# Kernel tuning notes

Measured on AMD Instinct MI355X. Metric: run time of the kernel, lower is better.

The kernel has to match this reference:

```python
import jax, jax.numpy as jnp
import numpy as np

N, IN_DIM, HIDDEN, L = 20000, 128, 256, 6
ALPHA = 0.1
EPS = 1e-5

def setup_inputs() -> dict:
    key = jax.random.key(0)
    ks = jax.random.split(key, 8)
    x = jax.random.normal(ks[0], (N, IN_DIM), dtype=jnp.float32)
    E = 320000
    src = jax.random.randint(ks[1], (E,), 0, N)
    dst = jax.random.randint(ks[2], (E,), 0, N)
    edge_index = jnp.stack([src, dst], axis=0)
    s = 1.0 / np.sqrt(IN_DIM)
    W_in = jax.random.normal(ks[3], (IN_DIM, HIDDEN), dtype=jnp.float32) * s
    b_in = jnp.zeros((HIDDEN,), dtype=jnp.float32)
    g_in = jnp.ones((HIDDEN,), dtype=jnp.float32)
    beta_in = jnp.zeros((HIDDEN,), dtype=jnp.float32)
    sc = 1.0 / np.sqrt(HIDDEN)
    Wc = jax.random.normal(ks[4], (L, HIDDEN, HIDDEN), dtype=jnp.float32) * sc
    bc = jnp.zeros((L, HIDDEN), dtype=jnp.float32)
    gc = jnp.ones((L, HIDDEN), dtype=jnp.float32)
    betac = jnp.zeros((L, HIDDEN), dtype=jnp.float32)
    return {"x": x, "edge_index": edge_index, "W_in": W_in, "b_in": b_in,
            "g_in": g_in, "beta_in": beta_in, "Wc": Wc, "bc": bc,
            "gc": gc, "betac": betac}

def _layer_norm(h, g, b):
    mu = jnp.mean(h, axis=-1, keepdims=True)
    var = jnp.mean((h - mu) ** 2, axis=-1, keepdims=True)
    return (h - mu) * jax.lax.rsqrt(var + EPS) * g + b

def _gcn_norm(edge_index, n):
    # add self loops (weight 1), symmetric normalization
    loop = jnp.arange(n, dtype=edge_index.dtype)
    row = jnp.concatenate([edge_index[0], loop])
    col = jnp.concatenate([edge_index[1], loop])
    w = jnp.ones((row.shape[0],), dtype=jnp.float32)
    deg = jax.ops.segment_sum(w, col, num_segments=n)
    dinv = jnp.where(deg > 0, jax.lax.rsqrt(deg), 0.0)
    norm = dinv[row] * w * dinv[col]
    return row, col, norm

def reference(x, edge_index, W_in, b_in, g_in, beta_in, Wc, bc, gc, betac):
    n = x.shape[0]
    row, col, norm = _gcn_norm(edge_index, n)
    # input block: Linear -> GELU -> LayerNorm (dropout = eval identity)
    h = _layer_norm(jax.nn.gelu(x @ W_in + b_in), g_in, beta_in)
    h0 = h
    xcur = h
    for l in range(L):
        z = xcur @ Wc[l]                              # [N, H]
        agg = jax.ops.segment_sum(z[row] * norm[:, None], col, num_segments=n)
        out = agg + bc[l]
        out = _layer_norm(jax.nn.gelu(out), gc[l], betac[l])
        hblend = (1.0 - ALPHA) * out + ALPHA * h0
        xcur = xcur + hblend
    return xcur
```

## Files before the change

### kernel.cpp

```cpp
#include <hip/hip_runtime.h>
#include <hip/hip_bf16.h>
#include <math.h>

#define HID 256
typedef __attribute__((ext_vector_type(8))) short s16x8;
typedef __attribute__((ext_vector_type(4))) float f32x4;

__device__ __forceinline__ ushort f2bf(float f){
    uint u = __float_as_uint(f);
    u += 0x7FFF + ((u>>16)&1);
    return (ushort)(u>>16);
}
__device__ __forceinline__ float bf2f(ushort b){
    return __uint_as_float(((uint)b)<<16);
}
__device__ __forceinline__ float4 bf4_to_f4(ushort4 u){
    return make_float4(bf2f(u.x), bf2f(u.y), bf2f(u.z), bf2f(u.w));
}

__device__ __forceinline__ float gelu_tanh(float x){
    float u = 0.7978845608028654f*(x + 0.044715f*x*x*x);
    float t = 1.0f - 2.0f/(1.0f + __expf(2.0f*u));
    return 0.5f*x*(1.0f+t);
}

__global__ void k_count(const int* __restrict__ dst, int* __restrict__ cnt, int E){
    int e = blockIdx.x*blockDim.x + threadIdx.x;
    if(e<E) atomicAdd(&cnt[dst[e]], 1);
}

__global__ __launch_bounds__(256) void k_scan1(const int* __restrict__ cnt,
    int* __restrict__ tsum, int* __restrict__ bsum, int N){
    __shared__ int sm[256];
    int t = threadIdx.x, b = blockIdx.x;
    int base = b*1024 + t*4;
    int c0=0,c1=0,c2=0,c3=0;
    if(base+3 < N){
        int4 c = *reinterpret_cast<const int4*>(&cnt[base]);
        c0=c.x; c1=c.y; c2=c.z; c3=c.w;
    }else{
        if(base  <N) c0=cnt[base];
        if(base+1<N) c1=cnt[base+1];
        if(base+2<N) c2=cnt[base+2];
        if(base+3<N) c3=cnt[base+3];
    }
    int s = c0+c1+c2+c3;
    sm[t]=s; __syncthreads();
    for(int off=1; off<256; off<<=1){
        int v = sm[t];
        int a = (t>=off)? sm[t-off] : 0;
        __syncthreads();
        sm[t] = v+a;
        __syncthreads();
    }
    tsum[b*256+t] = sm[t]-s;
    if(t==255) bsum[b] = sm[255];
}

__global__ void k_scan2(const int* __restrict__ bsum, int* __restrict__ boff,
    int* __restrict__ indptr, int B, int N){
    if(threadIdx.x==0 && blockIdx.x==0){
        int run=0;
        for(int i=0;i<B;i++){ boff[i]=run; run+=bsum[i]; }
        indptr[N]=run;
    }
}

__global__ __launch_bounds__(256) void k_scan3(const int* __restrict__ cnt,
    const int* __restrict__ tsum, const int* __restrict__ boff,
    int* __restrict__ indptr, int* __restrict__ cursor, float* __restrict__ dinv, int N){
    int t = threadIdx.x, b = blockIdx.x;
    int base = b*1024 + t*4;
    int run = boff[b] + tsum[b*256+t];
    #pragma unroll
    for(int i=0;i<4;i++){
        int idx = base+i;
        if(idx<N){
            int c = cnt[idx];
            indptr[idx]=run; cursor[idx]=run;
            dinv[idx] = rsqrtf((float)(c+1));
            run += c;
        }
    }
}

__global__ void k_fill(const int* __restrict__ src, const int* __restrict__ dst,
    int* __restrict__ cursor, int* __restrict__ csr, int E){
    int e = blockIdx.x*blockDim.x + threadIdx.x;
    if(e<E){
        int pos = atomicAdd(&cursor[dst[e]], 1);
        csr[pos] = src[e];
    }
}

__global__ void k_cvt(const float* __restrict__ in, ushort* __restrict__ out, int total4){
    int i = blockIdx.x*blockDim.x + threadIdx.x;
    if(i < total4){
        float4 v = reinterpret_cast<const float4*>(in)[i];
        ushort4 o; o.x=f2bf(v.x); o.y=f2bf(v.y); o.z=f2bf(v.z); o.w=f2bf(v.w);
        reinterpret_cast<ushort4*>(out)[i] = o;
    }
}

__global__ void k_cvt_win(const float* __restrict__ W, ushort* __restrict__ Wb){
    int i = blockIdx.x*blockDim.x + threadIdx.x;
    if(i >= 128*256) return;
    int k = i >> 8, n = i & 255;
    int kb = k>>5, hi=(k>>3)&3, ii=k&7;
    Wb[((kb*256+n)*4+hi)*8 + ii] = f2bf(W[i]);
}
__global__ void k_cvt_wc(const float* __restrict__ W, ushort* __restrict__ Wb){
    int i = blockIdx.x*blockDim.x + threadIdx.x;
    if(i >= 6*65536) return;
    int l = i >> 16;
    int k = (i>>8)&255, n = i&255;
    int kb = k>>5, hi=(k>>3)&3, ii=k&7;
    Wb[l*65536 + ((kb*256+n)*4+hi)*8 + ii] = f2bf(W[i]);
}

__global__ __launch_bounds__(256) void k_agg(const ushort* __restrict__ xsc,
    const int* __restrict__ indptr, const int* __restrict__ csr,
    const float* __restrict__ dinv, ushort* __restrict__ yb, int N)
{
    int wave = threadIdx.x>>6, lane = threadIdx.x&63;
    int n = blockIdx.x*4 + wave;
    if(n>=N) return;
    const ushort4* X4 = reinterpret_cast<const ushort4*>(xsc);
    float4 acc = bf4_to_f4(X4[(size_t)n*64+lane]);
    int e0 = indptr[n], e1 = indptr[n+1];
    int e = e0;
    for(; e+4<=e1; e+=4){
        int i0=csr[e], i1=csr[e+1], i2=csr[e+2], i3=csr[e+3];
        float4 v0 = bf4_to_f4(X4[(size_t)i0*64+lane]);
        float4 v1 = bf4_to_f4(X4[(size_t)i1*64+lane]);
        float4 v2 = bf4_to_f4(X4[(size_t)i2*64+lane]);
        float4 v3 = bf4_to_f4(X4[(size_t)i3*64+lane]);
        acc.x += (v0.x+v1.x)+(v2.x+v3.x);
        acc.y += (v0.y+v1.y)+(v2.y+v3.y);
        acc.z += (v0.z+v1.z)+(v2.z+v3.z);
        acc.w += (v0.w+v1.w)+(v2.w+v3.w);
    }
    for(; e<e1; e++){
        float4 v = bf4_to_f4(X4[(size_t)csr[e]*64+lane]);
        acc.x+=v.x; acc.y+=v.y; acc.z+=v.z; acc.w+=v.w;
    }
    float dn = dinv[n];
    ushort4 o; o.x=f2bf(dn*acc.x); o.y=f2bf(dn*acc.y); o.z=f2bf(dn*acc.z); o.w=f2bf(dn*acc.w);
    reinterpret_cast<ushort4*>(yb)[(size_t)n*64+lane] = o;
}

template<int K, bool INPUT>
__global__ __launch_bounds__(256) void k_gemm_fused(const ushort* __restrict__ A,
    const ushort* __restrict__ Wb,
    const float* __restrict__ bp, const float* __restrict__ gp, const float* __restrict__ bep,
    const float* __restrict__ dinv, ushort* __restrict__ h0b,
    float* __restrict__ xcur, ushort* __restrict__ xsc, int N)
{
    constexpr int KB = K/32;
    const int lane = threadIdx.x & 63;
    const int wc = threadIdx.x >> 6;
    const int lr = lane & 15;
    const int hi = lane >> 4;
    const int row0 = blockIdx.x*32;

    f32x4 acc[2][4];
    #pragma unroll
    for(int m=0;m<2;m++)
        #pragma unroll
        for(int n=0;n<4;n++){ acc[m][n].x=0.f; acc[m][n].y=0.f; acc[m][n].z=0.f; acc[m][n].w=0.f; }

    int r0 = row0 + lr;      if(r0 >= N) r0 = N-1;
    int r1 = row0 + 16 + lr; if(r1 >= N) r1 = N-1;
    const ushort* ap0 = A + (size_t)r0*K + hi*8;
    const ushort* ap1 = A + (size_t)r1*K + hi*8;
    const ushort* bpp = Wb + (wc*64 + lr)*32 + hi*8;

    s16x8 a0[2], a1[2], bb[2][4];
    a0[0] = *reinterpret_cast<const s16x8*>(ap0);
    a1[0] = *reinterpret_cast<const s16x8*>(ap1);
    #pragma unroll
    for(int nf=0;nf<4;nf++) bb[0][nf] = *reinterpret_cast<const s16x8*>(bpp + nf*512);

    #pragma unroll
    for(int kb=0; kb<KB; kb++){
        const int cur = kb&1, nxt = cur^1;
        if(kb+1 < KB){
            a0[nxt] = *reinterpret_cast<const s16x8*>(ap0 + (kb+1)*32);
            a1[nxt] = *reinterpret_cast<const s16x8*>(ap1 + (kb+1)*32);
            #pragma unroll
            for(int nf=0;nf<4;nf++)
                bb[nxt][nf] = *reinterpret_cast<const s16x8*>(bpp + (kb+1)*8192 + nf*512);
        }
        #pragma unroll
        for(int nf=0;nf<4;nf++){
            acc[0][nf] = __builtin_amdgcn_mfma_f32_16x16x32_bf16(a0[cur], bb[cur][nf], acc[0][nf], 0,0,0);
            acc[1][nf] = __builtin_amdgcn_mfma_f32_16x16x32_bf16(a1[cur], bb[cur][nf], acc[1][nf], 0,0,0);
        }
    }

    float bcv[4], gcv[4], bev[4];
    #pragma unroll
    for(int nf=0;nf<4;nf++){
        int col = wc*64 + nf*16 + lr;
        bcv[nf]=bp[col]; gcv[nf]=gp[col]; bev[nf]=bep[col];
    }
    __shared__ float sm1[32][4];
    __shared__ float sm2[32][4];
    #pragma unroll
    for(int m=0;m<2;m++){
        #pragma unroll
        for(int r=0;r<4;r++){
            float ls1=0.f, ls2=0.f;
            #pragma unroll
            for(int nf=0;nf<4;nf++){
                float t = gelu_tanh(acc[m][nf][r] + bcv[nf]);
                acc[m][nf][r] = t;
                ls1 += t; ls2 += t*t;
            }
            #pragma unroll
            for(int off=1; off<16; off<<=1){
                ls1 += __shfl_xor(ls1, off, 64);
                ls2 += __shfl_xor(ls2, off, 64);
            }
            if(lr==0){
                int row = m*16 + hi*4 + r;
                sm1[row][wc]=ls1; sm2[row][wc]=ls2;
            }
        }
    }
    __syncthreads();
    #pragma unroll
    for(int m=0;m<2;m++){
        #pragma unroll
        for(int r=0;r<4;r++){
            int row = m*16 + hi*4 + r;
            int grow = row0 + row;
            if(grow >= N) continue;
            float S1 = sm1[row][0]+sm1[row][1]+sm1[row][2]+sm1[row][3];
            float S2 = sm2[row][0]+sm2[row][1]+sm2[row][2]+sm2[row][3];
            float mu = S1*(1.0f/256.0f);
            float var = fmaxf(S2*(1.0f/256.0f) - mu*mu, 0.0f);
            float rs = rsqrtf(var + 1e-5f);
            float dv = dinv[grow];
            #pragma unroll
            for(int nf=0;nf<4;nf++){
                int col = wc*64 + nf*16 + lr;
                size_t idx = (size_t)grow*HID + col;
                float o = (acc[m][nf][r]-mu)*rs*gcv[nf] + bev[nf];
                if(INPUT){
                    h0b[idx] = f2bf(o);
                    xcur[idx] = o;
                    xsc[idx] = f2bf(dv*o);
                }else{
                    float h = bf2f(h0b[idx]);
                    float xc = xcur[idx] + 0.9f*o + 0.1f*h;
                    xcur[idx] = xc;
                    xsc[idx] = f2bf(dv*xc);
                }
            }
        }
    }
}

extern "C" void kernel_launch(void* const* d_in, const int* in_sizes, int n_in,
                              void* d_out, int out_size, void* d_ws, size_t ws_size,
                              hipStream_t stream){
    const float* x     = (const float*)d_in[0];
    const int*   ei    = (const int*)d_in[1];
    const float* W_in  = (const float*)d_in[2];
    const float* b_in  = (const float*)d_in[3];
    const float* g_in  = (const float*)d_in[4];
    const float* be_in = (const float*)d_in[5];
    const float* Wc    = (const float*)d_in[6];
    const float* bc    = (const float*)d_in[7];
    const float* gc    = (const float*)d_in[8];
    const float* bec   = (const float*)d_in[9];
    const int N = in_sizes[0]/128;
    const int E = in_sizes[1]/2;
    const int* src = ei;
    const int* dst = ei + E;
    float* xcur = (float*)d_out;
    const int B = (N+1023)/1024;

    char* w = (char*)d_ws;
    ushort* xsc  = (ushort*)w; w += (size_t)N*HID*2;
    ushort* yb   = (ushort*)w; w += (size_t)N*HID*2;
    ushort* h0b  = (ushort*)w; w += (size_t)N*HID*2;
    ushort* xin  = (ushort*)w; w += (size_t)N*128*2;
    ushort* wbin = (ushort*)w; w += (size_t)128*256*2;
    ushort* wbc  = (ushort*)w; w += (size_t)6*65536*2;
    float* dinv  = (float*)w;  w += (size_t)N*4;
    int* cnt     = (int*)w;    w += (size_t)N*4;
    int* cursor  = (int*)w;    w += (size_t)N*4;
    int* csr     = (int*)w;    w += (size_t)E*4;
    int* indptr  = (int*)w;    w += (size_t)(N+1)*4;
    int* tsum    = (int*)w;    w += (size_t)B*256*4;
    int* bsum    = (int*)w;    w += (size_t)B*4;
    int* boff    = (int*)w;    w += (size_t)B*4;

    hipMemsetAsync(cnt, 0, (size_t)N*4, stream);
    k_count<<<(E+255)/256,256,0,stream>>>(dst,cnt,E);
    k_scan1<<<B,256,0,stream>>>(cnt, tsum, bsum, N);
    k_scan2<<<1,64,0,stream>>>(bsum, boff, indptr, B, N);
    k_scan3<<<B,256,0,stream>>>(cnt, tsum, boff, indptr, cursor, dinv, N);
    k_fill<<<(E+255)/256,256,0,stream>>>(src,dst,cursor,csr,E);

    k_cvt<<<((N*128/4)+255)/256,256,0,stream>>>(x, xin, N*128/4);
    k_cvt_win<<<(128*256+255)/256,256,0,stream>>>(W_in, wbin);
    k_cvt_wc<<<(6*65536+255)/256,256,0,stream>>>(Wc, wbc);

    const int GB = (N+31)/32;
    k_gemm_fused<128,true><<<GB,256,0,stream>>>(xin, wbin, b_in, g_in, be_in,
                                                dinv, h0b, xcur, xsc, N);
    for(int l=0;l<6;l++){
        k_agg<<<(N+3)/4,256,0,stream>>>(xsc, indptr, csr, dinv, yb, N);
        k_gemm_fused<256,false><<<GB,256,0,stream>>>(yb, wbc+(size_t)l*65536,
            bc+(size_t)l*HID, gc+(size_t)l*HID, bec+(size_t)l*HID,
            dinv, h0b, xcur, xsc, N);
    }
}
```

Measured before the change: 361.7 us.

## Fuse neighbor aggregation into the per-layer GEMM via LDS staging

Merges the CSR gather-aggregation kernel into the layer GEMM. Each block aggregates its 32 rows into swizzled shared memory, then runs MFMA directly from LDS, with ping-pong feature buffers between layers. The fp32-to-bf16 conversion of the input features is also folded into the input GEMM. This removes the intermediate aggregated-feature round trip through global memory, seven launches and one conversion pass. In exchange, far fewer waves are available to hide the latency of the irregular gather, since each wave now walks 8 nodes serially.

```diff
diff --git a/kernel.cpp b/kernel.cpp
--- a/kernel.cpp
+++ b/kernel.cpp
@@ -93,15 +93,6 @@
     }
 }
 
-__global__ void k_cvt(const float* __restrict__ in, ushort* __restrict__ out, int total4){
-    int i = blockIdx.x*blockDim.x + threadIdx.x;
-    if(i < total4){
-        float4 v = reinterpret_cast<const float4*>(in)[i];
-        ushort4 o; o.x=f2bf(v.x); o.y=f2bf(v.y); o.z=f2bf(v.z); o.w=f2bf(v.w);
-        reinterpret_cast<ushort4*>(out)[i] = o;
-    }
-}
-
 __global__ void k_cvt_win(const float* __restrict__ W, ushort* __restrict__ Wb){
     int i = blockIdx.x*blockDim.x + threadIdx.x;
     if(i >= 128*256) return;
@@ -118,94 +109,20 @@
     Wb[l*65536 + ((kb*256+n)*4+hi)*8 + ii] = f2bf(W[i]);
 }
 
-__global__ __launch_bounds__(256) void k_agg(const ushort* __restrict__ xsc,
-    const int* __restrict__ indptr, const int* __restrict__ csr,
-    const float* __restrict__ dinv, ushort* __restrict__ yb, int N)
-{
-    int wave = threadIdx.x>>6, lane = threadIdx.x&63;
-    int n = blockIdx.x*4 + wave;
-    if(n>=N) return;
-    const ushort4* X4 = reinterpret_cast<const ushort4*>(xsc);
-    float4 acc = bf4_to_f4(X4[(size_t)n*64+lane]);
-    int e0 = indptr[n], e1 = indptr[n+1];
-    int e = e0;
-    for(; e+4<=e1; e+=4){
-        int i0=csr[e], i1=csr[e+1], i2=csr[e+2], i3=csr[e+3];
-        float4 v0 = bf4_to_f4(X4[(size_t)i0*64+lane]);
-        float4 v1 = bf4_to_f4(X4[(size_t)i1*64+lane]);
-        float4 v2 = bf4_to_f4(X4[(size_t)i2*64+lane]);
-        float4 v3 = bf4_to_f4(X4[(size_t)i3*64+lane]);
-        acc.x += (v0.x+v1.x)+(v2.x+v3.x);
-        acc.y += (v0.y+v1.y)+(v2.y+v3.y);
-        acc.z += (v0.z+v1.z)+(v2.z+v3.z);
-        acc.w += (v0.w+v1.w)+(v2.w+v3.w);
-    }
-    for(; e<e1; e++){
-        float4 v = bf4_to_f4(X4[(size_t)csr[e]*64+lane]);
-        acc.x+=v.x; acc.y+=v.y; acc.z+=v.z; acc.w+=v.w;
-    }
-    float dn = dinv[n];
-    ushort4 o; o.x=f2bf(dn*acc.x); o.y=f2bf(dn*acc.y); o.z=f2bf(dn*acc.z); o.w=f2bf(dn*acc.w);
-    reinterpret_cast<ushort4*>(yb)[(size_t)n*64+lane] = o;
-}
-
-template<int K, bool INPUT>
-__global__ __launch_bounds__(256) void k_gemm_fused(const ushort* __restrict__ A,
-    const ushort* __restrict__ Wb,
+template<bool INPUT>
+__device__ __forceinline__ void epilogue(f32x4 (&acc)[2][4],
     const float* __restrict__ bp, const float* __restrict__ gp, const float* __restrict__ bep,
     const float* __restrict__ dinv, ushort* __restrict__ h0b,
-    float* __restrict__ xcur, ushort* __restrict__ xsc, int N)
+    float* __restrict__ xcur, ushort* __restrict__ xs_out,
+    int row0, int wc, int lr, int hi, int N,
+    float (*sm1)[4], float (*sm2)[4])
 {
-    constexpr int KB = K/32;
-    const int lane = threadIdx.x & 63;
-    const int wc = threadIdx.x >> 6;
-    const int lr = lane & 15;
-    const int hi = lane >> 4;
-    const int row0 = blockIdx.x*32;
-
-    f32x4 acc[2][4];
-    #pragma unroll
-    for(int m=0;m<2;m++)
-        #pragma unroll
-        for(int n=0;n<4;n++){ acc[m][n].x=0.f; acc[m][n].y=0.f; acc[m][n].z=0.f; acc[m][n].w=0.f; }
-
-    int r0 = row0 + lr;      if(r0 >= N) r0 = N-1;
-    int r1 = row0 + 16 + lr; if(r1 >= N) r1 = N-1;
-    const ushort* ap0 = A + (size_t)r0*K + hi*8;
-    const ushort* ap1 = A + (size_t)r1*K + hi*8;
-    const ushort* bpp = Wb + (wc*64 + lr)*32 + hi*8;
-
-    s16x8 a0[2], a1[2], bb[2][4];
-    a0[0] = *reinterpret_cast<const s16x8*>(ap0);
-    a1[0] = *reinterpret_cast<const s16x8*>(ap1);
-    #pragma unroll
-    for(int nf=0;nf<4;nf++) bb[0][nf] = *reinterpret_cast<const s16x8*>(bpp + nf*512);
-
-    #pragma unroll
-    for(int kb=0; kb<KB; kb++){
-        const int cur = kb&1, nxt = cur^1;
-        if(kb+1 < KB){
-            a0[nxt] = *reinterpret_cast<const s16x8*>(ap0 + (kb+1)*32);
-            a1[nxt] = *reinterpret_cast<const s16x8*>(ap1 + (kb+1)*32);
-            #pragma unroll
-            for(int nf=0;nf<4;nf++)
-                bb[nxt][nf] = *reinterpret_cast<const s16x8*>(bpp + (kb+1)*8192 + nf*512);
-        }
-        #pragma unroll
-        for(int nf=0;nf<4;nf++){
-            acc[0][nf] = __builtin_amdgcn_mfma_f32_16x16x32_bf16(a0[cur], bb[cur][nf], acc[0][nf], 0,0,0);
-            acc[1][nf] = __builtin_amdgcn_mfma_f32_16x16x32_bf16(a1[cur], bb[cur][nf], acc[1][nf], 0,0,0);
-        }
-    }
-
     float bcv[4], gcv[4], bev[4];
     #pragma unroll
     for(int nf=0;nf<4;nf++){
         int col = wc*64 + nf*16 + lr;
         bcv[nf]=bp[col]; gcv[nf]=gp[col]; bev[nf]=bep[col];
     }
-    __shared__ float sm1[32][4];
-    __shared__ float sm2[32][4];
     #pragma unroll
     for(int m=0;m<2;m++){
         #pragma unroll
@@ -250,16 +167,144 @@
                 if(INPUT){
                     h0b[idx] = f2bf(o);
                     xcur[idx] = o;
-                    xsc[idx] = f2bf(dv*o);
+                    xs_out[idx] = f2bf(dv*o);
                 }else{
                     float h = bf2f(h0b[idx]);
                     float xc = xcur[idx] + 0.9f*o + 0.1f*h;
                     xcur[idx] = xc;
-                    xsc[idx] = f2bf(dv*xc);
+                    xs_out[idx] = f2bf(dv*xc);
                 }
             }
         }
     }
+}
+
+__global__ __launch_bounds__(256) void k_gemm_in(const float* __restrict__ X,
+    const ushort* __restrict__ Wb,
+    const float* __restrict__ bp, const float* __restrict__ gp, const float* __restrict__ bep,
+    const float* __restrict__ dinv, ushort* __restrict__ h0b,
+    float* __restrict__ xcur, ushort* __restrict__ xs_out, int N)
+{
+    const int lane = threadIdx.x & 63;
+    const int wc = threadIdx.x >> 6;
+    const int lr = lane & 15;
+    const int hi = lane >> 4;
+    const int row0 = blockIdx.x*32;
+    __shared__ float sm1[32][4];
+    __shared__ float sm2[32][4];
+
+    f32x4 acc[2][4];
+    #pragma unroll
+    for(int m=0;m<2;m++)
+        #pragma unroll
+        for(int n=0;n<4;n++){ acc[m][n].x=0.f; acc[m][n].y=0.f; acc[m][n].z=0.f; acc[m][n].w=0.f; }
+
+    int r0 = row0 + lr;      if(r0 >= N) r0 = N-1;
+    int r1 = row0 + 16 + lr; if(r1 >= N) r1 = N-1;
+    const float* xp0 = X + (size_t)r0*128 + hi*8;
+    const float* xp1 = X + (size_t)r1*128 + hi*8;
+    const ushort* bpp = Wb + (wc*64 + lr)*32 + hi*8;
+
+    #pragma unroll
+    for(int kb=0; kb<4; kb++){
+        float4 p0a = *reinterpret_cast<const float4*>(xp0 + kb*32);
+        float4 p0b = *reinterpret_cast<const float4*>(xp0 + kb*32 + 4);
+        float4 p1a = *reinterpret_cast<const float4*>(xp1 + kb*32);
+        float4 p1b = *reinterpret_cast<const float4*>(xp1 + kb*32 + 4);
+        s16x8 a0, a1;
+        a0[0]=(short)f2bf(p0a.x); a0[1]=(short)f2bf(p0a.y); a0[2]=(short)f2bf(p0a.z); a0[3]=(short)f2bf(p0a.w);
+        a0[4]=(short)f2bf(p0b.x); a0[5]=(short)f2bf(p0b.y); a0[6]=(short)f2bf(p0b.z); a0[7]=(short)f2bf(p0b.w);
+        a1[0]=(short)f2bf(p1a.x); a1[1]=(short)f2bf(p1a.y); a1[2]=(short)f2bf(p1a.z); a1[3]=(short)f2bf(p1a.w);
+        a1[4]=(short)f2bf(p1b.x); a1[5]=(short)f2bf(p1b.y); a1[6]=(short)f2bf(p1b.z); a1[7]=(short)f2bf(p1b.w);
+        #pragma unroll
+        for(int nf=0;nf<4;nf++){
+            s16x8 b = *reinterpret_cast<const s16x8*>(bpp + kb*8192 + nf*512);
+            acc[0][nf] = __builtin_amdgcn_mfma_f32_16x16x32_bf16(a0, b, acc[0][nf], 0,0,0);
+            acc[1][nf] = __builtin_amdgcn_mfma_f32_16x16x32_bf16(a1, b, acc[1][nf], 0,0,0);
+        }
+    }
+    epilogue<true>(acc, bp, gp, bep, dinv, h0b, xcur, xs_out, row0, wc, lr, hi, N, sm1, sm2);
+}
+
+__global__ __launch_bounds__(256) void k_conv(const ushort* __restrict__ xs_in,
+    const ushort* __restrict__ Wb,
+    const int* __restrict__ indptr, const int* __restrict__ csr,
+    const float* __restrict__ dinv,
+    const float* __restrict__ bp, const float* __restrict__ gp, const float* __restrict__ bep,
+    ushort* __restrict__ h0b, float* __restrict__ xcur,
+    ushort* __restrict__ xs_out, int N)
+{
+    __shared__ ushort yls[32*256];
+    __shared__ float sm1[32][4];
+    __shared__ float sm2[32][4];
+    const int lane = threadIdx.x & 63;
+    const int wc = threadIdx.x >> 6;
+    const int lr = lane & 15;
+    const int hi = lane >> 4;
+    const int row0 = blockIdx.x*32;
+
+    const ushort4* X4 = reinterpret_cast<const ushort4*>(xs_in);
+    char* ybase = (char*)yls;
+    #pragma unroll 1
+    for(int i=0;i<8;i++){
+        int li = wc*8 + i;
+        int n = row0 + li;
+        if(n >= N) n = N-1;
+        float4 acc = bf4_to_f4(X4[(size_t)n*64 + lane]);
+        int e0 = indptr[n], e1 = indptr[n+1];
+        int e = e0;
+        for(; e+4<=e1; e+=4){
+            int i0=csr[e], i1=csr[e+1], i2=csr[e+2], i3=csr[e+3];
+            float4 v0 = bf4_to_f4(X4[(size_t)i0*64+lane]);
+            float4 v1 = bf4_to_f4(X4[(size_t)i1*64+lane]);
+            float4 v2 = bf4_to_f4(X4[(size_t)i2*64+lane]);
+            float4 v3 = bf4_to_f4(X4[(size_t)i3*64+lane]);
+            acc.x += (v0.x+v1.x)+(v2.x+v3.x);
+            acc.y += (v0.y+v1.y)+(v2.y+v3.y);
+            acc.z += (v0.z+v1.z)+(v2.z+v3.z);
+            acc.w += (v0.w+v1.w)+(v2.w+v3.w);
+        }
+        for(; e<e1; e++){
+            float4 v = bf4_to_f4(X4[(size_t)csr[e]*64+lane]);
+            acc.x+=v.x; acc.y+=v.y; acc.z+=v.z; acc.w+=v.w;
+        }
+        float dn = dinv[n];
+        ushort4 o; o.x=f2bf(dn*acc.x); o.y=f2bf(dn*acc.y); o.z=f2bf(dn*acc.z); o.w=f2bf(dn*acc.w);
+        *reinterpret_cast<ushort4*>(ybase + li*512 + ((lane*8) ^ ((li&7)<<4))) = o;
+    }
+    __syncthreads();
+
+    f32x4 acc[2][4];
+    #pragma unroll
+    for(int m=0;m<2;m++)
+        #pragma unroll
+        for(int n=0;n<4;n++){ acc[m][n].x=0.f; acc[m][n].y=0.f; acc[m][n].z=0.f; acc[m][n].w=0.f; }
+
+    const ushort* bpp = Wb + (wc*64 + lr)*32 + hi*8;
+    s16x8 bb[2][4];
+    #pragma unroll
+    for(int nf=0;nf<4;nf++) bb[0][nf] = *reinterpret_cast<const s16x8*>(bpp + nf*512);
+
+    const int sws = (lr&7)<<4;
+    #pragma unroll
+    for(int kb=0; kb<8; kb++){
+        const int cur = kb&1, nxt = cur^1;
+        if(kb < 7){
+            #pragma unroll
+            for(int nf=0;nf<4;nf++)
+                bb[nxt][nf] = *reinterpret_cast<const s16x8*>(bpp + (kb+1)*8192 + nf*512);
+        }
+        int cb = kb*64 + hi*16;
+        s16x8 a0 = *reinterpret_cast<const s16x8*>(ybase + lr*512        + (cb ^ sws));
+        s16x8 a1 = *reinterpret_cast<const s16x8*>(ybase + (16+lr)*512   + (cb ^ sws));
+        #pragma unroll
+        for(int nf=0;nf<4;nf++){
+            acc[0][nf] = __builtin_amdgcn_mfma_f32_16x16x32_bf16(a0, bb[cur][nf], acc[0][nf], 0,0,0);
+            acc[1][nf] = __builtin_amdgcn_mfma_f32_16x16x32_bf16(a1, bb[cur][nf], acc[1][nf], 0,0,0);
+        }
+    }
+    __syncthreads();
+    epilogue<false>(acc, bp, gp, bep, dinv, h0b, xcur, xs_out, row0, wc, lr, hi, N, sm1, sm2);
 }
 
 extern "C" void kernel_launch(void* const* d_in, const int* in_sizes, int n_in,
@@ -283,10 +328,9 @@
     const int B = (N+1023)/1024;
 
     char* w = (char*)d_ws;
-    ushort* xsc  = (ushort*)w; w += (size_t)N*HID*2;
-    ushort* yb   = (ushort*)w; w += (size_t)N*HID*2;
+    ushort* xs0  = (ushort*)w; w += (size_t)N*HID*2;
+    ushort* xs1  = (ushort*)w; w += (size_t)N*HID*2;
     ushort* h0b  = (ushort*)w; w += (size_t)N*HID*2;
-    ushort* xin  = (ushort*)w; w += (size_t)N*128*2;
     ushort* wbin = (ushort*)w; w += (size_t)128*256*2;
     ushort* wbc  = (ushort*)w; w += (size_t)6*65536*2;
     float* dinv  = (float*)w;  w += (size_t)N*4;
@@ -298,24 +342,24 @@
     int* bsum    = (int*)w;    w += (size_t)B*4;
     int* boff    = (int*)w;    w += (size_t)B*4;
 
-    hipMemsetAsync(cnt, 0, (size_t)N*4, stream);
+    (void)hipMemsetAsync(cnt, 0, (size_t)N*4, stream);
     k_count<<<(E+255)/256,256,0,stream>>>(dst,cnt,E);
     k_scan1<<<B,256,0,stream>>>(cnt, tsum, bsum, N);
     k_scan2<<<1,64,0,stream>>>(bsum, boff, indptr, B, N);
     k_scan3<<<B,256,0,stream>>>(cnt, tsum, boff, indptr, cursor, dinv, N);
     k_fill<<<(E+255)/256,256,0,stream>>>(src,dst,cursor,csr,E);
 
-    k_cvt<<<((N*128/4)+255)/256,256,0,stream>>>(x, xin, N*128/4);
     k_cvt_win<<<(128*256+255)/256,256,0,stream>>>(W_in, wbin);
     k_cvt_wc<<<(6*65536+255)/256,256,0,stream>>>(Wc, wbc);
 
     const int GB = (N+31)/32;
-    k_gemm_fused<128,true><<<GB,256,0,stream>>>(xin, wbin, b_in, g_in, be_in,
-                                                dinv, h0b, xcur, xsc, N);
+    k_gemm_in<<<GB,256,0,stream>>>(x, wbin, b_in, g_in, be_in, dinv, h0b, xcur, xs0, N);
+    ushort* xsA = xs0;
+    ushort* xsB = xs1;
     for(int l=0;l<6;l++){
-        k_agg<<<(N+3)/4,256,0,stream>>>(xsc, indptr, csr, dinv, yb, N);
-        k_gemm_fused<256,false><<<GB,256,0,stream>>>(yb, wbc+(size_t)l*65536,
+        k_conv<<<GB,256,0,stream>>>(xsA, wbc+(size_t)l*65536, indptr, csr, dinv,
             bc+(size_t)l*HID, gc+(size_t)l*HID, bec+(size_t)l*HID,
-            dinv, h0b, xcur, xsc, N);
-    }
-}
+            h0b, xcur, xsB, N);
+        ushort* t = xsA; xsA = xsB; xsB = t;
+    }
+}
```

New measurement: 410.4 us. +13.5%, slower.

## Fuse input conversion into GEMM, halve GEMM row tile, unroll aggregation by eight

Applied to the files above, without the earlier changes.

Drops the separate fp32-to-bf16 conversion kernel for x; the input GEMM now reads fp32 rows and converts them in registers. Both fused GEMM kernels now handle 16 rows per block instead of 32, which doubles the grid size and reuses each weight fragment load across fewer rows, with the epilogue moved into a shared helper. The aggregation loop issues eight gathers at a time instead of four to put more loads in flight. Smaller tiles increase weight traffic per row, and the wider unroll adds register pressure.

```diff
diff --git a/kernel.cpp b/kernel.cpp
--- a/kernel.cpp
+++ b/kernel.cpp
@@ -93,15 +93,6 @@
     }
 }
 
-__global__ void k_cvt(const float* __restrict__ in, ushort* __restrict__ out, int total4){
-    int i = blockIdx.x*blockDim.x + threadIdx.x;
-    if(i < total4){
-        float4 v = reinterpret_cast<const float4*>(in)[i];
-        ushort4 o; o.x=f2bf(v.x); o.y=f2bf(v.y); o.z=f2bf(v.z); o.w=f2bf(v.w);
-        reinterpret_cast<ushort4*>(out)[i] = o;
-    }
-}
-
 __global__ void k_cvt_win(const float* __restrict__ W, ushort* __restrict__ Wb){
     int i = blockIdx.x*blockDim.x + threadIdx.x;
     if(i >= 128*256) return;
@@ -129,7 +120,19 @@
     float4 acc = bf4_to_f4(X4[(size_t)n*64+lane]);
     int e0 = indptr[n], e1 = indptr[n+1];
     int e = e0;
-    for(; e+4<=e1; e+=4){
+    for(; e+8<=e1; e+=8){
+        int idx[8];
+        #pragma unroll
+        for(int q=0;q<8;q++) idx[q]=csr[e+q];
+        float4 v[8];
+        #pragma unroll
+        for(int q=0;q<8;q++) v[q]=bf4_to_f4(X4[(size_t)idx[q]*64+lane]);
+        #pragma unroll
+        for(int q=0;q<8;q++){
+            acc.x+=v[q].x; acc.y+=v[q].y; acc.z+=v[q].z; acc.w+=v[q].w;
+        }
+    }
+    if(e+4<=e1){
         int i0=csr[e], i1=csr[e+1], i2=csr[e+2], i3=csr[e+3];
         float4 v0 = bf4_to_f4(X4[(size_t)i0*64+lane]);
         float4 v1 = bf4_to_f4(X4[(size_t)i1*64+lane]);
@@ -139,6 +142,7 @@
         acc.y += (v0.y+v1.y)+(v2.y+v3.y);
         acc.z += (v0.z+v1.z)+(v2.z+v3.z);
         acc.w += (v0.w+v1.w)+(v2.w+v3.w);
+        e += 4;
     }
     for(; e<e1; e++){
         float4 v = bf4_to_f4(X4[(size_t)csr[e]*64+lane]);
@@ -149,117 +153,149 @@
     reinterpret_cast<ushort4*>(yb)[(size_t)n*64+lane] = o;
 }
 
-template<int K, bool INPUT>
+template<bool INPUT>
+__device__ __forceinline__ void epilogue16(f32x4 (&acc)[4],
+    const float* __restrict__ bp, const float* __restrict__ gp, const float* __restrict__ bep,
+    const float* __restrict__ dinv, ushort* __restrict__ h0b,
+    float* __restrict__ xcur, ushort* __restrict__ xs_out,
+    int row0, int wc, int lr, int hi, int N,
+    float (*sm1)[4], float (*sm2)[4])
+{
+    float bcv[4], gcv[4], bev[4];
+    #pragma unroll
+    for(int nf=0;nf<4;nf++){
+        int col = wc*64 + nf*16 + lr;
+        bcv[nf]=bp[col]; gcv[nf]=gp[col]; bev[nf]=bep[col];
+    }
+    #pragma unroll
+    for(int r=0;r<4;r++){
+        float ls1=0.f, ls2=0.f;
+        #pragma unroll
+        for(int nf=0;nf<4;nf++){
+            float t = gelu_tanh(acc[nf][r] + bcv[nf]);
+            acc[nf][r] = t;
+            ls1 += t; ls2 += t*t;
+        }
+        #pragma unroll
+        for(int off=1; off<16; off<<=1){
+            ls1 += __shfl_xor(ls1, off, 64);
+            ls2 += __shfl_xor(ls2, off, 64);
+        }
+        if(lr==0){
+            int row = hi*4 + r;
+            sm1[row][wc]=ls1; sm2[row][wc]=ls2;
+        }
+    }
+    __syncthreads();
+    #pragma unroll
+    for(int r=0;r<4;r++){
+        int row = hi*4 + r;
+        int grow = row0 + row;
+        if(grow >= N) continue;
+        float S1 = sm1[row][0]+sm1[row][1]+sm1[row][2]+sm1[row][3];
+        float S2 = sm2[row][0]+sm2[row][1]+sm2[row][2]+sm2[row][3];
+        float mu = S1*(1.0f/256.0f);
+        float var = fmaxf(S2*(1.0f/256.0f) - mu*mu, 0.0f);
+        float rs = rsqrtf(var + 1e-5f);
+        float dv = dinv[grow];
+        #pragma unroll
+        for(int nf=0;nf<4;nf++){
+            int col = wc*64 + nf*16 + lr;
+            size_t idx = (size_t)grow*HID + col;
+            float o = (acc[nf][r]-mu)*rs*gcv[nf] + bev[nf];
+            if(INPUT){
+                h0b[idx] = f2bf(o);
+                xcur[idx] = o;
+                xs_out[idx] = f2bf(dv*o);
+            }else{
+                float h = bf2f(h0b[idx]);
+                float xc = xcur[idx] + 0.9f*o + 0.1f*h;
+                xcur[idx] = xc;
+                xs_out[idx] = f2bf(dv*xc);
+            }
+        }
+    }
+}
+
+__global__ __launch_bounds__(256) void k_gemm_in(const float* __restrict__ X,
+    const ushort* __restrict__ Wb,
+    const float* __restrict__ bp, const float* __restrict__ gp, const float* __restrict__ bep,
+    const float* __restrict__ dinv, ushort* __restrict__ h0b,
+    float* __restrict__ xcur, ushort* __restrict__ xs_out, int N)
+{
+    const int lane = threadIdx.x & 63;
+    const int wc = threadIdx.x >> 6;
+    const int lr = lane & 15;
+    const int hi = lane >> 4;
+    const int row0 = blockIdx.x*16;
+    __shared__ float sm1[16][4];
+    __shared__ float sm2[16][4];
+
+    f32x4 acc[4];
+    #pragma unroll
+    for(int n=0;n<4;n++){ acc[n].x=0.f; acc[n].y=0.f; acc[n].z=0.f; acc[n].w=0.f; }
+
+    int r0 = row0 + lr; if(r0 >= N) r0 = N-1;
+    const float* xp0 = X + (size_t)r0*128 + hi*8;
+    const ushort* bpp = Wb + (wc*64 + lr)*32 + hi*8;
+
+    #pragma unroll
+    for(int kb=0; kb<4; kb++){
+        float4 p0a = *reinterpret_cast<const float4*>(xp0 + kb*32);
+        float4 p0b = *reinterpret_cast<const float4*>(xp0 + kb*32 + 4);
+        s16x8 a0;
+        a0[0]=(short)f2bf(p0a.x); a0[1]=(short)f2bf(p0a.y); a0[2]=(short)f2bf(p0a.z); a0[3]=(short)f2bf(p0a.w);
+        a0[4]=(short)f2bf(p0b.x); a0[5]=(short)f2bf(p0b.y); a0[6]=(short)f2bf(p0b.z); a0[7]=(short)f2bf(p0b.w);
+        #pragma unroll
+        for(int nf=0;nf<4;nf++){
+            s16x8 b = *reinterpret_cast<const s16x8*>(bpp + kb*8192 + nf*512);
+            acc[nf] = __builtin_amdgcn_mfma_f32_16x16x32_bf16(a0, b, acc[nf], 0,0,0);
+        }
+    }
+    epilogue16<true>(acc, bp, gp, bep, dinv, h0b, xcur, xs_out, row0, wc, lr, hi, N, sm1, sm2);
+}
+
 __global__ __launch_bounds__(256) void k_gemm_fused(const ushort* __restrict__ A,
     const ushort* __restrict__ Wb,
     const float* __restrict__ bp, const float* __restrict__ gp, const float* __restrict__ bep,
     const float* __restrict__ dinv, ushort* __restrict__ h0b,
-    float* __restrict__ xcur, ushort* __restrict__ xsc, int N)
+    float* __restrict__ xcur, ushort* __restrict__ xs_out, int N)
 {
-    constexpr int KB = K/32;
     const int lane = threadIdx.x & 63;
     const int wc = threadIdx.x >> 6;
     const int lr = lane & 15;
     const int hi = lane >> 4;
-    const int row0 = blockIdx.x*32;
-
-    f32x4 acc[2][4];
-    #pragma unroll
-    for(int m=0;m<2;m++)
-        #pragma unroll
-        for(int n=0;n<4;n++){ acc[m][n].x=0.f; acc[m][n].y=0.f; acc[m][n].z=0.f; acc[m][n].w=0.f; }
-
-    int r0 = row0 + lr;      if(r0 >= N) r0 = N-1;
-    int r1 = row0 + 16 + lr; if(r1 >= N) r1 = N-1;
-    const ushort* ap0 = A + (size_t)r0*K + hi*8;
-    const ushort* ap1 = A + (size_t)r1*K + hi*8;
+    const int row0 = blockIdx.x*16;
+    __shared__ float sm1[16][4];
+    __shared__ float sm2[16][4];
+
+    f32x4 acc[4];
+    #pragma unroll
+    for(int n=0;n<4;n++){ acc[n].x=0.f; acc[n].y=0.f; acc[n].z=0.f; acc[n].w=0.f; }
+
+    int r0 = row0 + lr; if(r0 >= N) r0 = N-1;
+    const ushort* ap0 = A + (size_t)r0*256 + hi*8;
     const ushort* bpp = Wb + (wc*64 + lr)*32 + hi*8;
 
-    s16x8 a0[2], a1[2], bb[2][4];
+    s16x8 a0[2], bb[2][4];
     a0[0] = *reinterpret_cast<const s16x8*>(ap0);
-    a1[0] = *reinterpret_cast<const s16x8*>(ap1);
     #pragma unroll
     for(int nf=0;nf<4;nf++) bb[0][nf] = *reinterpret_cast<const s16x8*>(bpp + nf*512);
 
     #pragma unroll
-    for(int kb=0; kb<KB; kb++){
+    for(int kb=0; kb<8; kb++){
         const int cur = kb&1, nxt = cur^1;
-        if(kb+1 < KB){
+        if(kb < 7){
             a0[nxt] = *reinterpret_cast<const s16x8*>(ap0 + (kb+1)*32);
-            a1[nxt] = *reinterpret_cast<const s16x8*>(ap1 + (kb+1)*32);
             #pragma unroll
             for(int nf=0;nf<4;nf++)
                 bb[nxt][nf] = *reinterpret_cast<const s16x8*>(bpp + (kb+1)*8192 + nf*512);
         }
         #pragma unroll
-        for(int nf=0;nf<4;nf++){
-            acc[0][nf] = __builtin_amdgcn_mfma_f32_16x16x32_bf16(a0[cur], bb[cur][nf], acc[0][nf], 0,0,0);
-            acc[1][nf] = __builtin_amdgcn_mfma_f32_16x16x32_bf16(a1[cur], bb[cur][nf], acc[1][nf], 0,0,0);
-        }
-    }
-
-    float bcv[4], gcv[4], bev[4];
-    #pragma unroll
-    for(int nf=0;nf<4;nf++){
-        int col = wc*64 + nf*16 + lr;
-        bcv[nf]=bp[col]; gcv[nf]=gp[col]; bev[nf]=bep[col];
-    }
-    __shared__ float sm1[32][4];
-    __shared__ float sm2[32][4];
-    #pragma unroll
-    for(int m=0;m<2;m++){
-        #pragma unroll
-        for(int r=0;r<4;r++){
-            float ls1=0.f, ls2=0.f;
-            #pragma unroll
-            for(int nf=0;nf<4;nf++){
-                float t = gelu_tanh(acc[m][nf][r] + bcv[nf]);
-                acc[m][nf][r] = t;
-                ls1 += t; ls2 += t*t;
-            }
-            #pragma unroll
-            for(int off=1; off<16; off<<=1){
-                ls1 += __shfl_xor(ls1, off, 64);
-                ls2 += __shfl_xor(ls2, off, 64);
-            }
-            if(lr==0){
-                int row = m*16 + hi*4 + r;
-                sm1[row][wc]=ls1; sm2[row][wc]=ls2;
-            }
-        }
-    }
-    __syncthreads();
-    #pragma unroll
-    for(int m=0;m<2;m++){
-        #pragma unroll
-        for(int r=0;r<4;r++){
-            int row = m*16 + hi*4 + r;
-            int grow = row0 + row;
-            if(grow >= N) continue;
-            float S1 = sm1[row][0]+sm1[row][1]+sm1[row][2]+sm1[row][3];
-            float S2 = sm2[row][0]+sm2[row][1]+sm2[row][2]+sm2[row][3];
-            float mu = S1*(1.0f/256.0f);
-            float var = fmaxf(S2*(1.0f/256.0f) - mu*mu, 0.0f);
-            float rs = rsqrtf(var + 1e-5f);
-            float dv = dinv[grow];
-            #pragma unroll
-            for(int nf=0;nf<4;nf++){
-                int col = wc*64 + nf*16 + lr;
-                size_t idx = (size_t)grow*HID + col;
-                float o = (acc[m][nf][r]-mu)*rs*gcv[nf] + bev[nf];
-                if(INPUT){
-                    h0b[idx] = f2bf(o);
-                    xcur[idx] = o;
-                    xsc[idx] = f2bf(dv*o);
-                }else{
-                    float h = bf2f(h0b[idx]);
-                    float xc = xcur[idx] + 0.9f*o + 0.1f*h;
-                    xcur[idx] = xc;
-                    xsc[idx] = f2bf(dv*xc);
-                }
-            }
-        }
-    }
+        for(int nf=0;nf<4;nf++)
+            acc[nf] = __builtin_amdgcn_mfma_f32_16x16x32_bf16(a0[cur], bb[cur][nf], acc[nf], 0,0,0);
+    }
+    epilogue16<false>(acc, bp, gp, bep, dinv, h0b, xcur, xs_out, row0, wc, lr, hi, N, sm1, sm2);
 }
 
 extern "C" void kernel_launch(void* const* d_in, const int* in_sizes, int n_in,
@@ -286,7 +322,6 @@
     ushort* xsc  = (ushort*)w; w += (size_t)N*HID*2;
     ushort* yb   = (ushort*)w; w += (size_t)N*HID*2;
     ushort* h0b  = (ushort*)w; w += (size_t)N*HID*2;
-    ushort* xin  = (ushort*)w; w += (size_t)N*128*2;
     ushort* wbin = (ushort*)w; w += (size_t)128*256*2;
     ushort* wbc  = (ushort*)w; w += (size_t)6*65536*2;
     float* dinv  = (float*)w;  w += (size_t)N*4;
@@ -298,23 +333,21 @@
     int* bsum    = (int*)w;    w += (size_t)B*4;
     int* boff    = (int*)w;    w += (size_t)B*4;
 
-    hipMemsetAsync(cnt, 0, (size_t)N*4, stream);
+    (void)hipMemsetAsync(cnt, 0, (size_t)N*4, stream);
     k_count<<<(E+255)/256,256,0,stream>>>(dst,cnt,E);
     k_scan1<<<B,256,0,stream>>>(cnt, tsum, bsum, N);
     k_scan2<<<1,64,0,stream>>>(bsum, boff, indptr, B, N);
     k_scan3<<<B,256,0,stream>>>(cnt, tsum, boff, indptr, cursor, dinv, N);
     k_fill<<<(E+255)/256,256,0,stream>>>(src,dst,cursor,csr,E);
 
-    k_cvt<<<((N*128/4)+255)/256,256,0,stream>>>(x, xin, N*128/4);
     k_cvt_win<<<(128*256+255)/256,256,0,stream>>>(W_in, wbin);
     k_cvt_wc<<<(6*65536+255)/256,256,0,stream>>>(Wc, wbc);
 
-    const int GB = (N+31)/32;
-    k_gemm_fused<128,true><<<GB,256,0,stream>>>(xin, wbin, b_in, g_in, be_in,
-                                                dinv, h0b, xcur, xsc, N);
+    const int GB = (N+15)/16;
+    k_gemm_in<<<GB,256,0,stream>>>(x, wbin, b_in, g_in, be_in, dinv, h0b, xcur, xsc, N);
     for(int l=0;l<6;l++){
         k_agg<<<(N+3)/4,256,0,stream>>>(xsc, indptr, csr, dinv, yb, N);
-        k_gemm_fused<256,false><<<GB,256,0,stream>>>(yb, wbc+(size_t)l*65536,
+        k_gemm_fused<<<GB,256,0,stream>>>(yb, wbc+(size_t)l*65536,
             bc+(size_t)l*HID, gc+(size_t)l*HID, bec+(size_t)l*HID,
             dinv, h0b, xcur, xsc, N);
     }
```

New measurement: 351.7 us. -2.8%, faster.
